# Optimization experiments

Hardware: AMD Instinct MI355X
Metric: run time of the kernel (lower is better)

The kernel has to match this reference:

```python
import jax, jax.numpy as jnp
import numpy as np

DIM = 256
HEADS = 8
B, T, D, H, W = 2, 8, 16, 16, 16


def _mha(x, wqkv, bqkv, wo, bo):
    # x: [M, S, F]; standard self-attention (q=k=v=x), LoRA rank 0.
    M, S, F = x.shape
    hd = F // HEADS
    qkv = jnp.einsum('msf,kfg->kmsg', x, wqkv) + bqkv[:, None, None, :]  # [3,M,S,F]
    q, k, v = qkv
    q = q.reshape(M, S, HEADS, hd).transpose(0, 2, 1, 3)  # [M,Hh,S,hd]
    k = k.reshape(M, S, HEADS, hd).transpose(0, 2, 1, 3)
    v = v.reshape(M, S, HEADS, hd).transpose(0, 2, 1, 3)
    scores = jnp.einsum('mhsd,mhtd->mhst', q, k) / jnp.sqrt(jnp.asarray(hd, x.dtype))
    attn = jax.nn.softmax(scores, axis=-1)
    out = jnp.einsum('mhst,mhtd->mhsd', attn, v)
    out = out.transpose(0, 2, 1, 3).reshape(M, S, F)
    return out @ wo + bo


def _make_params(key, name_suffix):
    k1, k2 = jax.random.split(key)
    s = 1.0 / np.sqrt(DIM)
    return {
        f'wqkv_{name_suffix}': jax.random.normal(k1, (3, DIM, DIM), jnp.float32) * s,
        f'bqkv_{name_suffix}': jnp.zeros((3, DIM), jnp.float32),
        f'wo_{name_suffix}': jax.random.normal(k2, (DIM, DIM), jnp.float32) * s,
        f'bo_{name_suffix}': jnp.zeros((DIM,), jnp.float32),
    }


def setup_inputs() -> dict:
    key = jax.random.key(0)
    ks = jax.random.split(key, 5)
    inp = {'x': jax.random.normal(ks[0], (B, T, D * H * W, DIM), jnp.float32)}
    for k, ax in zip(ks[1:], ['t', 'd', 'h', 'w']):
        inp.update(_make_params(k, ax))
    inp['grid_d'] = D
    inp['grid_h'] = H
    inp['grid_w'] = W
    return inp


def reference(x, wqkv_t, bqkv_t, wo_t, bo_t,
              wqkv_d, bqkv_d, wo_d, bo_d,
              wqkv_h, bqkv_h, wo_h, bo_h,
              wqkv_w, bqkv_w, wo_w, bo_w,
              grid_d, grid_h, grid_w):
    b, t, n, f = x.shape
    d, h, w = grid_d, grid_h, grid_w
    x = x.reshape(b, t, d, h, w, f)
    if t > 1:
        xt = x.transpose(0, 2, 3, 4, 1, 5).reshape(b * d * h * w, t, f)
        xt = _mha(xt, wqkv_t, bqkv_t, wo_t, bo_t)
        xt = xt.reshape(b, d, h, w, t, f).transpose(0, 4, 1, 2, 3, 5)
        x = x + xt
    xd = x.transpose(0, 1, 3, 4, 2, 5).reshape(b * t * h * w, d, f)
    xd = _mha(xd, wqkv_d, bqkv_d, wo_d, bo_d)
    xd = xd.reshape(b, t, h, w, d, f).transpose(0, 1, 4, 2, 3, 5)
    xh = x.transpose(0, 1, 2, 4, 3, 5).reshape(b * t * d * w, h, f)
    xh = _mha(xh, wqkv_h, bqkv_h, wo_h, bo_h)
    xh = xh.reshape(b, t, d, w, h, f).transpose(0, 1, 2, 4, 3, 5)
    xw = x.reshape(b * t * d * h, w, f)
    xw = _mha(xw, wqkv_w, bqkv_w, wo_w, bo_w)
    xw = xw.reshape(b, t, d, h, w, f)
    x_comb = x + xd + xh + xw
    return x_comb.reshape(b, t, d * h * w, f)
```

## Files before the change

kernel.cpp:

```cpp
#include <hip/hip_runtime.h>

typedef __attribute__((ext_vector_type(4))) float f32x4;
typedef __attribute__((ext_vector_type(8))) short s16x8;

__device__ __forceinline__ ushort f2bf(float f) {
  union { float f; uint u; } v; v.f = f;
  uint r = v.u + 0x7fffu + ((v.u >> 16) & 1u);
  return (ushort)(r >> 16);
}

__device__ __forceinline__ void glds16(const void* g, void* l) {
  __builtin_amdgcn_global_load_lds(
      (const __attribute__((address_space(1))) uint*)g,
      (__attribute__((address_space(3))) uint*)l, 16, 0, 0);
}

__device__ __forceinline__ int asidx(int row, int col) {
  return row*256 + ((((col>>3) ^ ((row&7)<<2)))<<3) + (col&7);
}
__device__ __forceinline__ int scridx(int row, int col) {
  return row*32 + ((((col>>3) ^ ((row>>2)&3)))<<3) + (col&7);
}

struct WSrc { const float* p[8]; };

__global__ __launch_bounds__(256) void prep_weights(WSrc s, ushort* wq, ushort* wo) {
  int mm = blockIdx.x >> 6;
  int t  = blockIdx.x & 63;
  int a = mm >> 2, sub = mm & 3;
  const float* src = (sub < 3) ? (s.p[a*2] + sub*65536) : s.p[a*2+1];
  ushort*      dst = (sub < 3) ? (wq + (a*3 + sub)*65536) : (wo + a*65536);
  int gt = (t >> 3) * 32, ft = (t & 7) * 32;
  __shared__ float tile[32][33];
  int lx = threadIdx.x & 31, ly = threadIdx.x >> 5;
#pragma unroll
  for (int i = 0; i < 4; i++)
    tile[ly + i*8][lx] = src[(ft + ly + i*8)*256 + gt + lx];
  __syncthreads();
#pragma unroll
  for (int i = 0; i < 4; i++) {
    int n = gt + ly + i*8, col = ft + lx;
    dst[asidx(n, col)] = f2bf(tile[lx][ly + i*8]);
  }
}

template<int AXIS>
__device__ __forceinline__ int token_index(int blk, int row) {
  if (AXIS == 0) {
    int seq = blk*8 + (row >> 3);
    int t = row & 7;
    int b = seq >> 12, n = seq & 4095;
    return (b*8 + t)*4096 + n;
  } else {
    int sid = blk*4 + (row >> 4);
    int bt = sid >> 8, lo = sid & 255, r = row & 15;
    if (AXIS == 1) { int hh = lo >> 4, ww = lo & 15; return bt*4096 + r*256 + hh*16 + ww; }
    if (AXIS == 2) { int dd = lo >> 4, ww = lo & 15; return bt*4096 + dd*256 + r*16 + ww; }
    { int dd = lo >> 4, hh = lo & 15; return bt*4096 + dd*256 + hh*16 + r; }
  }
}

#define PUB_BARRIER() do { \
    __builtin_amdgcn_sched_barrier(0); \
    asm volatile("s_waitcnt lgkmcnt(0)" ::: "memory"); \
    __builtin_amdgcn_sched_barrier(0); \
    __builtin_amdgcn_s_barrier(); \
    __builtin_amdgcn_sched_barrier(0); } while (0)

template<int AXIS>
__global__ __launch_bounds__(512, 4) void axial_pass(
    const float* __restrict__ x0, const ushort* __restrict__ xb,
    const ushort* __restrict__ wqkvT, const float* __restrict__ bqkv,
    const ushort* __restrict__ woT, const float* __restrict__ bo,
    float* __restrict__ out, ushort* __restrict__ x1b) {

  __shared__ ushort Wbuf[2][8192];
  __shared__ ushort As[16384];
  __shared__ ushort Scr[4][2048];

  const int tid = threadIdx.x, blk = blockIdx.x;
  const int wv = tid >> 6, lane = tid & 63, llo = lane & 15, lhi = lane >> 4;
  const int pr = wv >> 1, half = wv & 1;
  const int rr = half*16 + llo;
  ushort* Qs = Scr[pr];
  ushort* Ks = Qs + 512;
  ushort* Vt = Qs + 1024;
  const f32x4 fzero = {0.f, 0.f, 0.f, 0.f};
  const s16x8 szero = {0,0,0,0,0,0,0,0};

  auto issue_stage = [&](int s) {
    const ushort* src = (s < 24) ? (wqkvT + (s % 3)*65536 + (s / 3)*8192)
                                 : (woT + (s - 24)*8192);
    const ushort* g = src + wv*1024 + lane*8;
    ushort* l = &Wbuf[s & 1][wv*1024];
    glds16(g, l);
    glds16(g + 512, l + 512);
  };

  issue_stage(0);
  issue_stage(1);

  {
    int row = tid >> 3, j = tid & 7;
    int tok = token_index<AXIS>(blk, row);
    if (AXIS == 0) {
      const float4* s4 = (const float4*)(x0 + (size_t)tok*256);
#pragma unroll
      for (int i = 0; i < 4; i++) {
        int c = j + 8*i;
        float4 v0 = s4[c*2], v1 = s4[c*2 + 1];
        s16x8 o;
        o[0] = (short)f2bf(v0.x); o[1] = (short)f2bf(v0.y);
        o[2] = (short)f2bf(v0.z); o[3] = (short)f2bf(v0.w);
        o[4] = (short)f2bf(v1.x); o[5] = (short)f2bf(v1.y);
        o[6] = (short)f2bf(v1.z); o[7] = (short)f2bf(v1.w);
        *(s16x8*)(As + asidx(row, c*8)) = o;
      }
    } else {
      const s16x8* s8 = (const s16x8*)(xb + (size_t)tok*256);
#pragma unroll
      for (int i = 0; i < 4; i++) {
        int c = j + 8*i;
        *(s16x8*)(As + asidx(row, c*8)) = s8[c];
      }
    }
  }
  {
    int row = half*16 + (lane >> 2);
    int cc = 2 + (lane & 1);
    *(s16x8*)(Vt + row*32 + ((cc ^ ((row>>2)&3))<<3)) = szero;
  }
  __syncthreads();

  s16x8 af[8];
  const int xrow = pr*16 + llo;
#pragma unroll
  for (int ks = 0; ks < 8; ks++)
    af[ks] = *(const s16x8*)(As + asidx(xrow, (ks*4 + lhi)*8));

  auto proj = [&](int sb) -> f32x4 {
    const ushort* buf = Wbuf[sb];
    f32x4 c = fzero;
#pragma unroll
    for (int ks = 0; ks < 8; ks++) {
      s16x8 bv = *(const s16x8*)(buf + rr*256 + ((((ks*4+lhi) ^ ((rr&7)<<2)))<<3));
      c = __builtin_amdgcn_mfma_f32_16x16x32_bf16(af[ks], bv, c, 0, 0, 0);
    }
    return c;
  };

#define STAGE_PRE() do { \
    asm volatile("s_waitcnt vmcnt(2)" ::: "memory"); \
    __builtin_amdgcn_sched_barrier(0); \
    __builtin_amdgcn_s_barrier(); \
    __builtin_amdgcn_sched_barrier(0); } while (0)
#define STAGE_POST(snext) do { \
    PUB_BARRIER(); \
    issue_stage(snext); } while (0)

#pragma unroll 1
  for (int h = 0; h < 8; h++) {
    STAGE_PRE();
    {
      f32x4 c = proj(0  + ((3*h) & 1));
      float bias = bqkv[0*256 + h*32 + rr];
#pragma unroll
      for (int r = 0; r < 4; r++)
        Qs[scridx(lhi*4 + r, rr)] = f2bf(c[r] + bias);
    }
    STAGE_POST(3*h + 2);
    STAGE_PRE();
    {
      f32x4 c = proj((3*h + 1) & 1);
      float bias = bqkv[1*256 + h*32 + rr];
#pragma unroll
      for (int r = 0; r < 4; r++)
        Ks[scridx(lhi*4 + r, rr)] = f2bf(c[r] + bias);
    }
    STAGE_POST(3*h + 3);
    STAGE_PRE();
    {
      f32x4 c = proj((3*h + 2) & 1);
      float bias = bqkv[2*256 + h*32 + rr];
#pragma unroll
      for (int r = 0; r < 4; r++)
        Vt[scridx(rr, lhi*4 + r)] = f2bf(c[r] + bias);

      s16x8 aq = *(const s16x8*)(Qs + scridx(llo, lhi*8));
      s16x8 bk = *(const s16x8*)(Ks + scridx(llo, lhi*8));
      f32x4 sc = __builtin_amdgcn_mfma_f32_16x16x32_bf16(aq, bk, fzero, 0, 0, 0);

      PUB_BARRIER();

#pragma unroll
      for (int r = 0; r < 4; r++) {
        float s = sc[r] * 0.17677669529663689f;
        if (AXIS == 0) {
          int srow = lhi*4 + r;
          if ((srow >> 3) != (llo >> 3)) s = -1e30f;
        }
        float mx = s;
        mx = fmaxf(mx, __shfl_xor(mx, 1));
        mx = fmaxf(mx, __shfl_xor(mx, 2));
        mx = fmaxf(mx, __shfl_xor(mx, 4));
        mx = fmaxf(mx, __shfl_xor(mx, 8));
        float e = __expf(s - mx);
        float sm = e;
        sm += __shfl_xor(sm, 1);
        sm += __shfl_xor(sm, 2);
        sm += __shfl_xor(sm, 4);
        sm += __shfl_xor(sm, 8);
        Ks[scridx(lhi*4 + r, llo)] = f2bf(e * __builtin_amdgcn_rcpf(sm));
      }
      s16x8 ap = *(const s16x8*)(Ks + scridx(llo, lhi*8));
      s16x8 bv = *(const s16x8*)(Vt + scridx(rr, lhi*8));
      f32x4 o = __builtin_amdgcn_mfma_f32_16x16x32_bf16(ap, bv, fzero, 0, 0, 0);
#pragma unroll
      for (int r = 0; r < 4; r++)
        As[asidx(pr*16 + lhi*4 + r, h*32 + rr)] = f2bf(o[r]);
    }
    STAGE_POST(3*h + 4);
  }

  f32x4 acc[8];
#pragma unroll
  for (int st = 0; st < 8; st++) {
    if (st == 7) { asm volatile("s_waitcnt vmcnt(0)" ::: "memory"); }
    else         { asm volatile("s_waitcnt vmcnt(2)" ::: "memory"); }
    __builtin_amdgcn_sched_barrier(0);
    __builtin_amdgcn_s_barrier();
    __builtin_amdgcn_sched_barrier(0);
    if (st == 0) {
#pragma unroll
      for (int ks = 0; ks < 8; ks++)
        af[ks] = *(const s16x8*)(As + asidx(xrow, (ks*4 + lhi)*8));
#pragma unroll
      for (int i = 0; i < 8; i++) acc[i] = fzero;
    }
    {
      const ushort* buf = Wbuf[st & 1];
#pragma unroll
      for (int ks = 0; ks < 8; ks++) {
        s16x8 bw = *(const s16x8*)(buf + rr*256 + ((((ks*4+lhi) ^ ((rr&7)<<2)))<<3));
        acc[st] = __builtin_amdgcn_mfma_f32_16x16x32_bf16(af[ks], bw, acc[st], 0, 0, 0);
      }
    }
    if (st < 6) {
      PUB_BARRIER();
      issue_stage(26 + st);
    }
  }

#pragma unroll
  for (int r = 0; r < 4; r++) {
    int row = pr*16 + lhi*4 + r;
    int tok = token_index<AXIS>(blk, row);
    size_t base = (size_t)tok*256;
#pragma unroll
    for (int st = 0; st < 8; st++) {
      int f = st*32 + half*16 + llo;
      float v = acc[st][r] + bo[f];
      if (AXIS == 0) {
        v += x0[base + f];
        out[base + f] = v;
        x1b[base + f] = f2bf(v);
      } else {
        out[base + f] += v;
      }
    }
  }
#undef STAGE_PRE
#undef STAGE_POST
}

extern "C" void kernel_launch(void* const* d_in, const int* in_sizes, int n_in,
                              void* d_out, int out_size, void* d_ws, size_t ws_size,
                              hipStream_t stream) {
  const float* x = (const float*)d_in[0];
  ushort* wq  = (ushort*)d_ws;
  ushort* wo  = wq + 4*3*65536;
  ushort* x1b = wo + 4*65536;
  float* out = (float*)d_out;

  WSrc wsrc;
  wsrc.p[0] = (const float*)d_in[1];  wsrc.p[1] = (const float*)d_in[3];
  wsrc.p[2] = (const float*)d_in[5];  wsrc.p[3] = (const float*)d_in[7];
  wsrc.p[4] = (const float*)d_in[9];  wsrc.p[5] = (const float*)d_in[11];
  wsrc.p[6] = (const float*)d_in[13]; wsrc.p[7] = (const float*)d_in[15];
  prep_weights<<<dim3(1024), dim3(256), 0, stream>>>(wsrc, wq, wo);

  const float* bq_t = (const float*)d_in[2];  const float* bo_t = (const float*)d_in[4];
  const float* bq_d = (const float*)d_in[6];  const float* bo_d = (const float*)d_in[8];
  const float* bq_h = (const float*)d_in[10]; const float* bo_h = (const float*)d_in[12];
  const float* bq_w = (const float*)d_in[14]; const float* bo_w = (const float*)d_in[16];

  axial_pass<0><<<dim3(1024), dim3(512), 0, stream>>>(x, nullptr, wq + 0*3*65536, bq_t, wo + 0*65536, bo_t, out, x1b);
  axial_pass<1><<<dim3(1024), dim3(512), 0, stream>>>(nullptr, x1b, wq + 1*3*65536, bq_d, wo + 1*65536, bo_d, out, nullptr);
  axial_pass<2><<<dim3(1024), dim3(512), 0, stream>>>(nullptr, x1b, wq + 2*3*65536, bq_h, wo + 2*65536, bo_h, out, nullptr);
  axial_pass<3><<<dim3(1024), dim3(512), 0, stream>>>(nullptr, x1b, wq + 3*3*65536, bq_w, wo + 3*65536, bo_w, out, nullptr);
}
```

Baseline: 413.7 us.

## Collapse the weight-stage pipeline to one barrier per stage with single-stage prefetch

```diff
diff --git a/kernel.cpp b/kernel.cpp
--- a/kernel.cpp
+++ b/kernel.cpp
@@ -97,8 +97,16 @@
     glds16(g + 512, l + 512);
   };
 
+#define STAGE_SYNC(sn) do { \
+    __builtin_amdgcn_sched_barrier(0); \
+    asm volatile("s_waitcnt vmcnt(0) lgkmcnt(0)" ::: "memory"); \
+    __builtin_amdgcn_sched_barrier(0); \
+    __builtin_amdgcn_s_barrier(); \
+    __builtin_amdgcn_sched_barrier(0); \
+    if ((sn) < 32) issue_stage(sn); \
+  } while (0)
+
   issue_stage(0);
-  issue_stage(1);
 
   {
     int row = tid >> 3, j = tid & 7;
@@ -149,27 +157,17 @@
     return c;
   };
 
-#define STAGE_PRE() do { \
-    asm volatile("s_waitcnt vmcnt(2)" ::: "memory"); \
-    __builtin_amdgcn_sched_barrier(0); \
-    __builtin_amdgcn_s_barrier(); \
-    __builtin_amdgcn_sched_barrier(0); } while (0)
-#define STAGE_POST(snext) do { \
-    PUB_BARRIER(); \
-    issue_stage(snext); } while (0)
-
 #pragma unroll 1
   for (int h = 0; h < 8; h++) {
-    STAGE_PRE();
-    {
-      f32x4 c = proj(0  + ((3*h) & 1));
+    STAGE_SYNC(3*h + 1);
+    {
+      f32x4 c = proj((3*h) & 1);
       float bias = bqkv[0*256 + h*32 + rr];
 #pragma unroll
       for (int r = 0; r < 4; r++)
         Qs[scridx(lhi*4 + r, rr)] = f2bf(c[r] + bias);
     }
-    STAGE_POST(3*h + 2);
-    STAGE_PRE();
+    STAGE_SYNC(3*h + 2);
     {
       f32x4 c = proj((3*h + 1) & 1);
       float bias = bqkv[1*256 + h*32 + rr];
@@ -177,8 +175,7 @@
       for (int r = 0; r < 4; r++)
         Ks[scridx(lhi*4 + r, rr)] = f2bf(c[r] + bias);
     }
-    STAGE_POST(3*h + 3);
-    STAGE_PRE();
+    STAGE_SYNC(3*h + 3);
     {
       f32x4 c = proj((3*h + 2) & 1);
       float bias = bqkv[2*256 + h*32 + rr];
@@ -219,17 +216,12 @@
       for (int r = 0; r < 4; r++)
         As[asidx(pr*16 + lhi*4 + r, h*32 + rr)] = f2bf(o[r]);
     }
-    STAGE_POST(3*h + 4);
   }
 
   f32x4 acc[8];
-#pragma unroll
+#pragma unroll 1
   for (int st = 0; st < 8; st++) {
-    if (st == 7) { asm volatile("s_waitcnt vmcnt(0)" ::: "memory"); }
-    else         { asm volatile("s_waitcnt vmcnt(2)" ::: "memory"); }
-    __builtin_amdgcn_sched_barrier(0);
-    __builtin_amdgcn_s_barrier();
-    __builtin_amdgcn_sched_barrier(0);
+    STAGE_SYNC(25 + st);
     if (st == 0) {
 #pragma unroll
       for (int ks = 0; ks < 8; ks++)
@@ -244,10 +236,6 @@
         s16x8 bw = *(const s16x8*)(buf + rr*256 + ((((ks*4+lhi) ^ ((rr&7)<<2)))<<3));
         acc[st] = __builtin_amdgcn_mfma_f32_16x16x32_bf16(af[ks], bw, acc[st], 0, 0, 0);
       }
-    }
-    if (st < 6) {
-      PUB_BARRIER();
-      issue_stage(26 + st);
     }
   }
 
@@ -269,8 +257,7 @@
       }
     }
   }
-#undef STAGE_PRE
-#undef STAGE_POST
+#undef STAGE_SYNC
 }
 
 extern "C" void kernel_launch(void* const* d_in, const int* in_sizes, int n_in,
```

After: 435.8 us. 1.05x slower.
